# Kernel optimization log

Hardware: AMD Instinct MI355X
Metric: run time of the kernel (lower is better)

Reference implementation:

```python
import jax, jax.numpy as jnp
import numpy as np

NUM_UNITS = 64
NUM_NODES = 2048
COARSE_NODES = 256
INPUT_DIM = 1
BATCH = 64
AVG_DEGREE = 16


def _normalized_laplacian(adj):
    # A = A + I; L = D^-1/2 A^T D^-1/2 (matches scipy path in source)
    a = adj + np.eye(adj.shape[0], dtype=np.float64)
    d = a.sum(axis=1)
    d_inv_sqrt = np.power(d, -0.5)
    d_inv_sqrt[np.isinf(d_inv_sqrt)] = 0.0
    # (A @ D^-1/2).T @ D^-1/2 = A.T * d[:,None] * d[None,:]
    lap = a.T * d_inv_sqrt[:, None] * d_inv_sqrt[None, :]
    return lap.astype(np.float32)


def _random_adj(rng, n, deg):
    rows = np.repeat(np.arange(n), deg)
    cols = rng.integers(0, n, size=n * deg)
    a = np.zeros((n, n), dtype=np.float64)
    a[rows, cols] = 1.0
    a = np.maximum(a, a.T)  # symmetric
    np.fill_diagonal(a, 0.0)
    return a


def _xavier(key, shape):
    std = np.sqrt(2.0 / (shape[0] + shape[1]))
    return jax.random.normal(key, shape, dtype=jnp.float32) * std


def setup_inputs() -> dict:
    key = jax.random.key(0)
    ks = jax.random.split(key, 8)
    rng = np.random.default_rng(0)

    adj = jnp.asarray(_normalized_laplacian(_random_adj(rng, NUM_NODES, AVG_DEGREE)))
    adj1 = jnp.asarray(_normalized_laplacian(_random_adj(rng, COARSE_NODES, AVG_DEGREE)))
    # afc_mx in source is (num_nodes, coarse_nodes); afc = afc_mx.T, afct = afc_mx
    afc_mx = rng.random((NUM_NODES, COARSE_NODES)).astype(np.float32)
    afc = jnp.asarray(afc_mx.T)   # (C, N)
    afct = jnp.asarray(afc_mx)    # (N, C)

    in_size = INPUT_DIM + NUM_UNITS
    inputs = jax.random.normal(ks[0], (BATCH, NUM_NODES * INPUT_DIM), dtype=jnp.float32)
    state = jax.random.normal(ks[1], (BATCH, NUM_NODES * NUM_UNITS), dtype=jnp.float32)

    return {
        "inputs": inputs, "state": state,
        "adj": adj, "adj1": adj1, "afc": afc, "afct": afct,
        "w0": _xavier(ks[2], (in_size, 2 * NUM_UNITS)),
        "b0": jnp.zeros((2 * NUM_UNITS,), jnp.float32),
        "w1": _xavier(ks[3], (in_size, NUM_UNITS)),
        "b1": jnp.zeros((NUM_UNITS,), jnp.float32),
        "w01": _xavier(ks[4], (in_size, 2 * NUM_UNITS)),
        "b01": jnp.zeros((2 * NUM_UNITS,), jnp.float32),
        "w11": _xavier(ks[5], (in_size, NUM_UNITS)),
        "b11": jnp.zeros((NUM_UNITS,), jnp.float32),
    }


def _gc(inputs, state, adj, adj1, afc, afct, w, b, wf, bf):
    B = inputs.shape[0]
    N, C = adj.shape[0], adj1.shape[0]
    x = jnp.concatenate([inputs.reshape(B, N, -1), state.reshape(B, N, -1)], axis=2)
    F = x.shape[2]
    x0 = x.transpose(1, 2, 0).reshape(N, F * B)          # (N, F*B)
    x0fc = afc @ x0                                      # (C, F*B)
    x1 = adj @ x0                                        # graph conv, fine graph
    x1fc = adj1 @ x0fc                                   # graph conv, coarse graph
    x1 = x1 + jax.nn.sigmoid(afct @ x0fc)                # cross term fine<-coarse
    x1fc = x1fc + jax.nn.sigmoid(afc @ x1)               # cross term coarse<-fine
    out = x1.reshape(N, F, B).transpose(2, 0, 1).reshape(-1, F) @ w + b
    outfc = x1fc.reshape(C, F, B).transpose(2, 0, 1).reshape(-1, F) @ wf + bf
    return out.reshape(B, N, -1), outfc.reshape(B, C, -1)


def reference(inputs, state, adj, adj1, afc, afct, w0, b0, w1, b1, w01, b01, w11, b11):
    B = inputs.shape[0]
    N, U = NUM_NODES, NUM_UNITS
    x1, _x1fc = _gc(inputs, state, adj, adj1, afc, afct, w0, b0, w01, b01)
    value = jax.nn.sigmoid(x1)                           # (B, N, 2U)
    r, u = value[..., :U], value[..., U:]
    r = r.reshape(B, N * U)
    u = u.reshape(B, N * U)
    c0, _c1 = _gc(inputs, r * state, adj, adj1, afc, afct, w1, b1, w11, b11)
    c = jnp.tanh(c0).reshape(B, N * U)
    new_state = u * state + (1.0 - u) * c
    return new_state
```

## Files before the change

kernel.cpp:

```cpp
#include <hip/hip_runtime.h>
#include <hip/hip_bf16.h>
#include <math.h>

#define N_NODES 2048
#define C_NODES 256
#define BATCH   64
#define UNITS   64
#define JS      4096
#define NX      4160
#define JSX     4224
#define NU      131072
#define XSTR    4160
#define CAP     192

typedef short  s16x8 __attribute__((ext_vector_type(8)));
typedef float  f32x4 __attribute__((ext_vector_type(4)));

__device__ __forceinline__ float sigmoidf_(float x) { return 1.0f / (1.0f + __expf(-x)); }

__device__ __forceinline__ float bfs2f(short s) {
    union { float f; unsigned u; } w; w.u = ((unsigned)(unsigned short)s) << 16; return w.f;
}
__device__ __forceinline__ short f2bfs(float f) {
    __hip_bfloat16 h = __float2bfloat16(f);
    short s; __builtin_memcpy(&s, &h, 2); return s;
}

__device__ __forceinline__ void gload_lds16(const void* g, void* l) {
    __builtin_amdgcn_global_load_lds(
        (const __attribute__((address_space(1))) void*)g,
        (__attribute__((address_space(3))) void*)l, 16, 0, 0);
}

__global__ __launch_bounds__(256) void cvt_split(const float* __restrict__ s,
                                                 __hip_bfloat16* __restrict__ dh,
                                                 __hip_bfloat16* __restrict__ dl, int n)
{
    int stride = gridDim.x * 256;
    for (int i = blockIdx.x * 256 + threadIdx.x; i < n; i += stride) {
        float v = s[i];
        __hip_bfloat16 h = __float2bfloat16(v);
        dh[i] = h;
        dl[i] = __float2bfloat16(v - __bfloat162float(h));
    }
}

__global__ __launch_bounds__(256) void cvt_w(const float* __restrict__ w0,
                                             const float* __restrict__ w1,
                                             __hip_bfloat16* __restrict__ w0h, __hip_bfloat16* __restrict__ w0l,
                                             __hip_bfloat16* __restrict__ w1h, __hip_bfloat16* __restrict__ w1l)
{
    int stride = gridDim.x * 256;
    for (int e = blockIdx.x * 256 + threadIdx.x; e < 8192 + 4096; e += stride) {
        if (e < 8192) {
            int jj = e & 7, cell = e >> 3;
            int o = cell & 127, c = cell >> 7;
            float v = w0[(size_t)(1 + c * 8 + jj) * 128 + o];
            __hip_bfloat16 h = __float2bfloat16(v);
            w0h[e] = h; w0l[e] = __float2bfloat16(v - __bfloat162float(h));
        } else {
            int e2 = e - 8192;
            int jj = e2 & 7, cell = e2 >> 3;
            int o = cell & 63, c = cell >> 6;
            float v = w1[(size_t)(1 + c * 8 + jj) * 64 + o];
            __hip_bfloat16 h = __float2bfloat16(v);
            w1h[e2] = h; w1l[e2] = __float2bfloat16(v - __bfloat162float(h));
        }
    }
}

__global__ __launch_bounds__(256) void setup_ext(
    const float* __restrict__ inputs,
    __hip_bfloat16* __restrict__ xh, __hip_bfloat16* __restrict__ xl,
    __hip_bfloat16* __restrict__ fh, __hip_bfloat16* __restrict__ fl,
    __hip_bfloat16* __restrict__ X)
{
    int blk = blockIdx.x;
    if (blk < 64) {
        int b = blk;
        for (int n = threadIdx.x; n < N_NODES; n += 256) {
            float v = inputs[(size_t)b * N_NODES + n];
            __hip_bfloat16 h = __float2bfloat16(v);
            size_t o = (size_t)(JS + b) * N_NODES + n;
            xh[o] = h;
            xl[o] = __float2bfloat16(v - __bfloat162float(h));
            X[(size_t)n * XSTR + 4096 + b] = h;
        }
    } else {
        int r = NX + (blk - 64);
        __hip_bfloat16 z = __float2bfloat16(0.0f);
        for (int n = threadIdx.x; n < N_NODES; n += 256) {
            size_t o = (size_t)r * N_NODES + n;
            xh[o] = z; xl[o] = z;
        }
        for (int c = threadIdx.x; c < C_NODES; c += 256) {
            size_t o = (size_t)r * C_NODES + c;
            fh[o] = z; fl[o] = z;
        }
    }
}

__global__ __launch_bounds__(256) void build_csr(
    const float* __restrict__ adj,
    unsigned short* __restrict__ cols,
    float* __restrict__ vals,
    int* __restrict__ nnz)
{
    int row  = blockIdx.x * 4 + (threadIdx.x >> 6);
    int lane = threadIdx.x & 63;
    const float* a = adj + (size_t)row * N_NODES;
    int base = 0;
    for (int k0 = 0; k0 < N_NODES; k0 += 64) {
        float v = a[k0 + lane];
        unsigned long long m = __ballot(v != 0.0f);
        if (v != 0.0f) {
            int pos = base + __popcll(m & ((1ull << lane) - 1));
            if (pos < CAP) {
                cols[(size_t)row * CAP + pos] = (unsigned short)(k0 + lane);
                vals[(size_t)row * CAP + pos] = v;
            }
        }
        base += __popcll(m);
    }
    if (lane == 0) nnz[row] = base < CAP ? base : CAP;
}

__global__ __launch_bounds__(256) void build_x0sT(const float* __restrict__ st,
                                                  __hip_bfloat16* __restrict__ xh,
                                                  __hip_bfloat16* __restrict__ xl,
                                                  __hip_bfloat16* __restrict__ X)
{
    __shared__ float Ls[64 * 65];
    int n0 = blockIdx.x * 64;
    int b  = blockIdx.y;
    int t  = threadIdx.x;
    #pragma unroll
    for (int it = 0; it < 16; it++) {
        int idx = t + it * 256;
        int i = idx >> 6, u = idx & 63;
        float v = st[(size_t)b * NU + (size_t)(n0 + i) * 64 + u];
        Ls[i * 65 + u] = v;
        X[(size_t)(n0 + i) * XSTR + b * 64 + u] = __float2bfloat16(v);
    }
    __syncthreads();
    #pragma unroll
    for (int it = 0; it < 16; it++) {
        int idx = t + it * 256;
        int u = idx >> 6, i = idx & 63;
        float v = Ls[i * 65 + u];
        __hip_bfloat16 h = __float2bfloat16(v);
        size_t o = (size_t)(b * 64 + u) * N_NODES + n0 + i;
        xh[o] = h;
        xl[o] = __float2bfloat16(v - __bfloat162float(h));
    }
}

__global__ __launch_bounds__(256) void gemm1_split(
    const __hip_bfloat16* __restrict__ Ah, const __hip_bfloat16* __restrict__ Al,
    const __hip_bfloat16* __restrict__ Bh, const __hip_bfloat16* __restrict__ Bl,
    float* __restrict__ part)
{
    __shared__ __align__(16) __hip_bfloat16 AsH[4096];
    __shared__ __align__(16) __hip_bfloat16 AsL[4096];
    __shared__ __align__(16) __hip_bfloat16 BsH[4096];
    __shared__ __align__(16) __hip_bfloat16 BsL[4096];

    const int K = N_NODES;
    int tid  = threadIdx.x;
    int wave = tid >> 6, lane = tid & 63;
    int quad = lane >> 4, lr = lane & 15;
    int mBase = blockIdx.y * 64;
    int nBase = blockIdx.x * 64;
    int k0base = blockIdx.z * (K / 2);

    const __hip_bfloat16 *gAh[2], *gAl[2], *gBh[2], *gBl[2];
    __hip_bfloat16 *lAh[2], *lAl[2], *lBh[2], *lBl[2];
    #pragma unroll
    for (int ch = 0; ch < 2; ch++) {
        int cell = (wave * 2 + ch) * 64 + lane;
        int kb = cell >> 6, mm = cell & 63;
        size_t offA = (size_t)(mBase + mm) * K + k0base + kb * 8;
        size_t offB = (size_t)(nBase + mm) * K + k0base + kb * 8;
        gAh[ch] = Ah + offA; gAl[ch] = Al + offA;
        gBh[ch] = Bh + offB; gBl[ch] = Bl + offB;
        int lo = (wave * 2 + ch) * 512;
        lAh[ch] = AsH + lo; lAl[ch] = AsL + lo;
        lBh[ch] = BsH + lo; lBl[ch] = BsL + lo;
    }

    f32x4 acc[4];
    #pragma unroll
    for (int j = 0; j < 4; j++) { f32x4 z = {0.f,0.f,0.f,0.f}; acc[j] = z; }

    for (int k0 = 0; k0 < K / 2; k0 += 64) {
        #pragma unroll
        for (int ch = 0; ch < 2; ch++) {
            gload_lds16(gAh[ch] + k0, lAh[ch]);
            gload_lds16(gAl[ch] + k0, lAl[ch]);
            gload_lds16(gBh[ch] + k0, lBh[ch]);
            gload_lds16(gBl[ch] + k0, lBl[ch]);
        }
        __syncthreads();
        const s16x8* AhV = (const s16x8*)AsH;
        const s16x8* AlV = (const s16x8*)AsL;
        const s16x8* BhV = (const s16x8*)BsH;
        const s16x8* BlV = (const s16x8*)BsL;
        #pragma unroll
        for (int ks = 0; ks < 2; ks++) {
            int kb = ks * 4 + quad;
            s16x8 ah = AhV[kb * 64 + wave * 16 + lr];
            s16x8 al = AlV[kb * 64 + wave * 16 + lr];
            s16x8 bh[4], bl[4];
            #pragma unroll
            for (int j = 0; j < 4; j++) {
                bh[j] = BhV[kb * 64 + j * 16 + lr];
                bl[j] = BlV[kb * 64 + j * 16 + lr];
            }
            #pragma unroll
            for (int j = 0; j < 4; j++) {
                acc[j] = __builtin_amdgcn_mfma_f32_16x16x32_bf16(ah, bh[j], acc[j], 0, 0, 0);
                acc[j] = __builtin_amdgcn_mfma_f32_16x16x32_bf16(ah, bl[j], acc[j], 0, 0, 0);
                acc[j] = __builtin_amdgcn_mfma_f32_16x16x32_bf16(al, bh[j], acc[j], 0, 0, 0);
            }
        }
        __syncthreads();
    }

    float* dst = part + (size_t)blockIdx.z * NX * C_NODES;
    #pragma unroll
    for (int j = 0; j < 4; j++)
        #pragma unroll
        for (int r = 0; r < 4; r++) {
            int row = mBase + wave * 16 + quad * 4 + r;
            int col = nBase + j * 16 + lr;
            dst[(size_t)row * C_NODES + col] = acc[j][r];
        }
}

__global__ __launch_bounds__(256) void reduce_split(const float* __restrict__ part,
                                                    __hip_bfloat16* __restrict__ oh,
                                                    __hip_bfloat16* __restrict__ ol, int n)
{
    int stride = gridDim.x * 256;
    for (int i = blockIdx.x * 256 + threadIdx.x; i < n; i += stride) {
        float v = part[i] + part[(size_t)n + i];
        __hip_bfloat16 h = __float2bfloat16(v);
        oh[i] = h;
        ol[i] = __float2bfloat16(v - __bfloat162float(h));
    }
}

__global__ __launch_bounds__(256, 2) void gemm_coarse(
    const __hip_bfloat16* __restrict__ Ah, const __hip_bfloat16* __restrict__ Al,
    const __hip_bfloat16* __restrict__ Bh, const __hip_bfloat16* __restrict__ Bl,
    __hip_bfloat16* __restrict__ OutH, __hip_bfloat16* __restrict__ OutL)
{
    __shared__ __align__(16) __hip_bfloat16 S1[8192];
    __shared__ __align__(16) __hip_bfloat16 S2[8192];
    __shared__ __align__(16) __hip_bfloat16 S3[8192];
    __shared__ __align__(16) __hip_bfloat16 S4[8192];

    int tid  = threadIdx.x;
    int wave = tid >> 6, lane = tid & 63;
    int quad = lane >> 4, lr = lane & 15;
    int wr = wave >> 1, wc = wave & 1;
    int mBase = blockIdx.y * 128, nBase = blockIdx.x * 128;

    int cellkb[4], cellmm[4];
    #pragma unroll
    for (int ch = 0; ch < 4; ch++) {
        int cell = (wave * 4 + ch) * 64 + lane;
        cellkb[ch] = cell >> 7;
        cellmm[ch] = cell & 127;
    }

    f32x4 acc[4][4];
    #pragma unroll
    for (int i = 0; i < 4; i++)
        #pragma unroll
        for (int j = 0; j < 4; j++) { f32x4 z = {0.f,0.f,0.f,0.f}; acc[i][j] = z; }

    for (int k0 = 0; k0 < C_NODES; k0 += 64) {
        #pragma unroll
        for (int ch = 0; ch < 4; ch++) {
            size_t offA = (size_t)(mBase + cellmm[ch]) * C_NODES + k0 + cellkb[ch] * 8;
            size_t offB = (size_t)(nBase + cellmm[ch]) * C_NODES + k0 + cellkb[ch] * 8;
            int lo = (wave * 4 + ch) * 512;
            gload_lds16(Ah + offA, S1 + lo);
            gload_lds16(Al + offA, S2 + lo);
            gload_lds16(Bh + offB, S3 + lo);
            gload_lds16(Bl + offB, S4 + lo);
        }
        __syncthreads();
        const s16x8* AhV = (const s16x8*)S1;
        const s16x8* AlV = (const s16x8*)S2;
        const s16x8* BhV = (const s16x8*)S3;
        const s16x8* BlV = (const s16x8*)S4;
        #pragma unroll
        for (int ks = 0; ks < 2; ks++) {
            int kb = ks * 4 + quad;
            s16x8 ah[4], al[4], bh[4], bl[4];
            #pragma unroll
            for (int i = 0; i < 4; i++) {
                int idx = kb * 128 + wr * 64 + i * 16 + lr;
                ah[i] = AhV[idx]; al[i] = AlV[idx];
            }
            #pragma unroll
            for (int j = 0; j < 4; j++) {
                int idx = kb * 128 + wc * 64 + j * 16 + lr;
                bh[j] = BhV[idx]; bl[j] = BlV[idx];
            }
            #pragma unroll
            for (int i = 0; i < 4; i++)
                #pragma unroll
                for (int j = 0; j < 4; j++) {
                    acc[i][j] = __builtin_amdgcn_mfma_f32_16x16x32_bf16(ah[i], bh[j], acc[i][j], 0, 0, 0);
                    acc[i][j] = __builtin_amdgcn_mfma_f32_16x16x32_bf16(ah[i], bl[j], acc[i][j], 0, 0, 0);
                    acc[i][j] = __builtin_amdgcn_mfma_f32_16x16x32_bf16(al[i], bh[j], acc[i][j], 0, 0, 0);
                }
        }
        __syncthreads();
    }

    #pragma unroll
    for (int i = 0; i < 4; i++)
        #pragma unroll
        for (int j = 0; j < 4; j++)
            #pragma unroll
            for (int r = 0; r < 4; r++) {
                int row = mBase + wr * 64 + i * 16 + quad * 4 + r;
                int col = nBase + wc * 64 + j * 16 + lr;
                float v = sigmoidf_(acc[i][j][r]);
                size_t idx = (size_t)row * JSX + col;
                __hip_bfloat16 h = __float2bfloat16(v);
                OutH[idx] = h;
                OutL[idx] = __float2bfloat16(v - __bfloat162float(h));
            }
}

__global__ __launch_bounds__(256) void spmm_add(
    const __hip_bfloat16* __restrict__ X,
    const unsigned short* __restrict__ cols,
    const float* __restrict__ vals,
    const int* __restrict__ nnz,
    __hip_bfloat16* __restrict__ OutH,
    __hip_bfloat16* __restrict__ OutL)
{
    int wave = threadIdx.x >> 6, lane = threadIdx.x & 63;
    int n  = blockIdx.x * 4 + wave;
    int jt = blockIdx.y;
    int cnt = nnz[n];
    const unsigned short* cp = cols + (size_t)n * CAP;
    const float*          vp = vals + (size_t)n * CAP;
    const short* Xs = (const short*)X;

    if (jt < 8) {
        int j0 = jt * 512 + lane * 8;
        float acc[8];
        #pragma unroll
        for (int e = 0; e < 8; e++) acc[e] = 0.f;
        int i = 0;
        for (; i + 4 <= cnt; i += 4) {
            int   c0 = cp[i+0], c1 = cp[i+1], c2 = cp[i+2], c3 = cp[i+3];
            float a0 = vp[i+0], a1 = vp[i+1], a2 = vp[i+2], a3 = vp[i+3];
            s16x8 x0 = *(const s16x8*)(Xs + (size_t)c0 * XSTR + j0);
            s16x8 x1 = *(const s16x8*)(Xs + (size_t)c1 * XSTR + j0);
            s16x8 x2 = *(const s16x8*)(Xs + (size_t)c2 * XSTR + j0);
            s16x8 x3 = *(const s16x8*)(Xs + (size_t)c3 * XSTR + j0);
            #pragma unroll
            for (int e = 0; e < 8; e++)
                acc[e] += a0 * bfs2f(x0[e]) + a1 * bfs2f(x1[e])
                        + a2 * bfs2f(x2[e]) + a3 * bfs2f(x3[e]);
        }
        for (; i < cnt; i++) {
            int c = cp[i]; float a = vp[i];
            s16x8 xv = *(const s16x8*)(Xs + (size_t)c * XSTR + j0);
            #pragma unroll
            for (int e = 0; e < 8; e++) acc[e] += a * bfs2f(xv[e]);
        }
        size_t o = (size_t)n * JSX + jt * 512 + lane * 8;
        s16x8 h = *(const s16x8*)((const short*)OutH + o);
        s16x8 l = *(const s16x8*)((const short*)OutL + o);
        s16x8 nh, nl;
        #pragma unroll
        for (int e = 0; e < 8; e++) {
            float v = bfs2f(h[e]) + bfs2f(l[e]) + acc[e];
            short hh = f2bfs(v);
            nh[e] = hh;
            nl[e] = f2bfs(v - bfs2f(hh));
        }
        *(s16x8*)((short*)OutH + o) = nh;
        *(s16x8*)((short*)OutL + o) = nl;
    } else {
        float acc = 0.f;
        for (int i = 0; i < cnt; i++) {
            int c = cp[i]; float a = vp[i];
            acc += a * bfs2f(Xs[(size_t)c * XSTR + 4096 + lane]);
        }
        size_t o = (size_t)n * JSX + JS + lane;
        float v = bfs2f(((const short*)OutH)[o]) + bfs2f(((const short*)OutL)[o]) + acc;
        short hh = f2bfs(v);
        ((short*)OutH)[o] = hh;
        ((short*)OutL)[o] = f2bfs(v - bfs2f(hh));
    }
}

__global__ __launch_bounds__(256) void head1_mfma(
    const __hip_bfloat16* __restrict__ x1h, const __hip_bfloat16* __restrict__ x1l,
    const __hip_bfloat16* __restrict__ Wh, const __hip_bfloat16* __restrict__ Wl,
    const float* __restrict__ w0, const float* __restrict__ b0,
    const float* __restrict__ state,
    __hip_bfloat16* __restrict__ xh, __hip_bfloat16* __restrict__ xl,
    __hip_bfloat16* __restrict__ u_buf,
    __hip_bfloat16* __restrict__ Xout)
{
    __shared__ __align__(16) __hip_bfloat16 XsH[8192];
    __shared__ __align__(16) __hip_bfloat16 XsL[8192];
    __shared__ __align__(16) __hip_bfloat16 WhS[8192];
    __shared__ __align__(16) __hip_bfloat16 WlS[8192];
    __shared__ float xinS[128];

    int n0 = blockIdx.x * 128;
    int b  = blockIdx.y;
    int tid = threadIdx.x;
    int wave = tid >> 6, lane = tid & 63;
    int quad = lane >> 4, lr = lane & 15;
    int wr = wave >> 1, wc = wave & 1;

    #pragma unroll
    for (int ch = 0; ch < 4; ch++) {
        int idx = (wave * 4 + ch) * 64 + lane;
        int c = idx >> 7, n = idx & 127;
        size_t gx = (size_t)(n0 + n) * JSX + b * 64 + c * 8;
        gload_lds16(x1h + gx, XsH + (wave * 4 + ch) * 512);
        gload_lds16(x1l + gx, XsL + (wave * 4 + ch) * 512);
        gload_lds16(Wh + (size_t)idx * 8, WhS + (wave * 4 + ch) * 512);
        gload_lds16(Wl + (size_t)idx * 8, WlS + (wave * 4 + ch) * 512);
    }
    if (tid < 128) {
        size_t o = (size_t)(n0 + tid) * JSX + JS + b;
        xinS[tid] = __bfloat162float(x1h[o]) + __bfloat162float(x1l[o]);
    }
    __syncthreads();

    f32x4 acc[4][4];
    #pragma unroll
    for (int i = 0; i < 4; i++)
        #pragma unroll
        for (int j = 0; j < 4; j++) { f32x4 z = {0.f,0.f,0.f,0.f}; acc[i][j] = z; }

    const s16x8* XhV = (const s16x8*)XsH;
    const s16x8* XlV = (const s16x8*)XsL;
    const s16x8* WhV = (const s16x8*)WhS;
    const s16x8* WlV = (const s16x8*)WlS;
    #pragma unroll
    for (int ks = 0; ks < 2; ks++) {
        int kb = ks * 4 + quad;
        s16x8 ah[4], al[4], bh[4], bl[4];
        #pragma unroll
        for (int i = 0; i < 4; i++) {
            int idx = kb * 128 + wr * 64 + i * 16 + lr;
            ah[i] = XhV[idx]; al[i] = XlV[idx];
        }
        #pragma unroll
        for (int j = 0; j < 4; j++) {
            int idx = kb * 128 + wc * 64 + j * 16 + lr;
            bh[j] = WhV[idx]; bl[j] = WlV[idx];
        }
        #pragma unroll
        for (int i = 0; i < 4; i++)
            #pragma unroll
            for (int j = 0; j < 4; j++) {
                acc[i][j] = __builtin_amdgcn_mfma_f32_16x16x32_bf16(ah[i], bh[j], acc[i][j], 0, 0, 0);
                acc[i][j] = __builtin_amdgcn_mfma_f32_16x16x32_bf16(ah[i], bl[j], acc[i][j], 0, 0, 0);
                acc[i][j] = __builtin_amdgcn_mfma_f32_16x16x32_bf16(al[i], bh[j], acc[i][j], 0, 0, 0);
            }
    }
    __syncthreads();

    __hip_bfloat16* trH = XsH;
    __hip_bfloat16* trL = XsL;
    __hip_bfloat16* trX = WhS;

    #pragma unroll
    for (int i = 0; i < 4; i++)
        #pragma unroll
        for (int j = 0; j < 4; j++)
            #pragma unroll
            for (int r = 0; r < 4; r++) {
                int n_loc = wr * 64 + i * 16 + quad * 4 + r;
                int o = wc * 64 + j * 16 + lr;
                float g = acc[i][j][r] + w0[o] * xinS[n_loc] + b0[o];
                float sg = sigmoidf_(g);
                if (wc == 0) {
                    float sv = state[(size_t)b * NU + (size_t)(n0 + n_loc) * 64 + o];
                    float rs = sg * sv;
                    __hip_bfloat16 h = __float2bfloat16(rs);
                    trH[o * 128 + n_loc] = h;
                    trL[o * 128 + n_loc] = __float2bfloat16(rs - __bfloat162float(h));
                    trX[n_loc * 64 + o] = h;
                } else {
                    u_buf[(size_t)b * NU + (size_t)(n0 + n_loc) * 64 + (o - 64)] = __float2bfloat16(sg);
                }
            }
    __syncthreads();

    {
        int row = tid >> 2, seg = tid & 3;
        const uint4* sh = (const uint4*)(trH + row * 128 + seg * 32);
        const uint4* sl = (const uint4*)(trL + row * 128 + seg * 32);
        uint4* dh = (uint4*)(xh + (size_t)(b * 64 + row) * N_NODES + n0 + seg * 32);
        uint4* dl = (uint4*)(xl + (size_t)(b * 64 + row) * N_NODES + n0 + seg * 32);
        #pragma unroll
        for (int q = 0; q < 4; q++) { dh[q] = sh[q]; dl[q] = sl[q]; }
    }
    {
        int row2 = tid >> 1, half = tid & 1;
        const uint4* s = (const uint4*)(trX + row2 * 64 + half * 32);
        uint4* d = (uint4*)(Xout + (size_t)(n0 + row2) * XSTR + b * 64 + half * 32);
        #pragma unroll
        for (int q = 0; q < 4; q++) d[q] = s[q];
    }
}

__global__ __launch_bounds__(256) void head2_mfma(
    const __hip_bfloat16* __restrict__ x1h, const __hip_bfloat16* __restrict__ x1l,
    const __hip_bfloat16* __restrict__ Wh, const __hip_bfloat16* __restrict__ Wl,
    const float* __restrict__ w1, const float* __restrict__ b1,
    const float* __restrict__ state, const __hip_bfloat16* __restrict__ u_buf,
    float* __restrict__ out)
{
    __shared__ __align__(16) __hip_bfloat16 XsH[8192];
    __shared__ __align__(16) __hip_bfloat16 XsL[8192];
    __shared__ __align__(16) __hip_bfloat16 WhS[4096];
    __shared__ __align__(16) __hip_bfloat16 WlS[4096];
    __shared__ float xinS[128];

    int n0 = blockIdx.x * 128;
    int b  = blockIdx.y;
    int tid = threadIdx.x;
    int wave = tid >> 6, lane = tid & 63;
    int quad = lane >> 4, lr = lane & 15;

    #pragma unroll
    for (int ch = 0; ch < 4; ch++) {
        int idx = (wave * 4 + ch) * 64 + lane;
        int c = idx >> 7, n = idx & 127;
        size_t gx = (size_t)(n0 + n) * JSX + b * 64 + c * 8;
        gload_lds16(x1h + gx, XsH + (wave * 4 + ch) * 512);
        gload_lds16(x1l + gx, XsL + (wave * 4 + ch) * 512);
    }
    #pragma unroll
    for (int ch = 0; ch < 2; ch++) {
        int idx = (wave * 2 + ch) * 64 + lane;
        gload_lds16(Wh + (size_t)idx * 8, WhS + (wave * 2 + ch) * 512);
        gload_lds16(Wl + (size_t)idx * 8, WlS + (wave * 2 + ch) * 512);
    }
    if (tid < 128) {
        size_t o = (size_t)(n0 + tid) * JSX + JS + b;
        xinS[tid] = __bfloat162float(x1h[o]) + __bfloat162float(x1l[o]);
    }
    __syncthreads();

    f32x4 acc[2][4];
    #pragma unroll
    for (int i = 0; i < 2; i++)
        #pragma unroll
        for (int j = 0; j < 4; j++) { f32x4 z = {0.f,0.f,0.f,0.f}; acc[i][j] = z; }

    const s16x8* XhV = (const s16x8*)XsH;
    const s16x8* XlV = (const s16x8*)XsL;
    const s16x8* WhV = (const s16x8*)WhS;
    const s16x8* WlV = (const s16x8*)WlS;
    #pragma unroll
    for (int ks = 0; ks < 2; ks++) {
        int kb = ks * 4 + quad;
        s16x8 ah[2], al[2], bh[4], bl[4];
        #pragma unroll
        for (int i = 0; i < 2; i++) {
            int idx = kb * 128 + wave * 32 + i * 16 + lr;
            ah[i] = XhV[idx]; al[i] = XlV[idx];
        }
        #pragma unroll
        for (int j = 0; j < 4; j++) {
            int idx = kb * 64 + j * 16 + lr;
            bh[j] = WhV[idx]; bl[j] = WlV[idx];
        }
        #pragma unroll
        for (int i = 0; i < 2; i++)
            #pragma unroll
            for (int j = 0; j < 4; j++) {
                acc[i][j] = __builtin_amdgcn_mfma_f32_16x16x32_bf16(ah[i], bh[j], acc[i][j], 0, 0, 0);
                acc[i][j] = __builtin_amdgcn_mfma_f32_16x16x32_bf16(ah[i], bl[j], acc[i][j], 0, 0, 0);
                acc[i][j] = __builtin_amdgcn_mfma_f32_16x16x32_bf16(al[i], bh[j], acc[i][j], 0, 0, 0);
            }
    }

    #pragma unroll
    for (int i = 0; i < 2; i++)
        #pragma unroll
        for (int j = 0; j < 4; j++)
            #pragma unroll
            for (int r = 0; r < 4; r++) {
                int n_loc = wave * 32 + i * 16 + quad * 4 + r;
                int o = j * 16 + lr;
                float g = acc[i][j][r] + w1[o] * xinS[n_loc] + b1[o];
                float c = tanhf(g);
                size_t sidx = (size_t)b * NU + (size_t)(n0 + n_loc) * 64 + o;
                float ug = __bfloat162float(u_buf[sidx]);
                float sv = state[sidx];
                out[sidx] = ug * sv + (1.0f - ug) * c;
            }
}

extern "C" void kernel_launch(void* const* d_in, const int* in_sizes, int n_in,
                              void* d_out, int out_size, void* d_ws, size_t ws_size,
                              hipStream_t stream)
{
    const float* inputs = (const float*)d_in[0];
    const float* state  = (const float*)d_in[1];
    const float* adj    = (const float*)d_in[2];
    const float* afc    = (const float*)d_in[4];
    const float* afct   = (const float*)d_in[5];
    const float* w0     = (const float*)d_in[6];
    const float* b0     = (const float*)d_in[7];
    const float* w1     = (const float*)d_in[8];
    const float* b1     = (const float*)d_in[9];

    float* out = (float*)d_out;

    char* p = (char*)d_ws;
    __hip_bfloat16* afc_h    = (__hip_bfloat16*)p; p += (size_t)C_NODES * N_NODES * 2;
    __hip_bfloat16* afc_l    = (__hip_bfloat16*)p; p += (size_t)C_NODES * N_NODES * 2;
    __hip_bfloat16* afct_h   = (__hip_bfloat16*)p; p += (size_t)N_NODES * C_NODES * 2;
    __hip_bfloat16* afct_l   = (__hip_bfloat16*)p; p += (size_t)N_NODES * C_NODES * 2;
    __hip_bfloat16* w0T_h    = (__hip_bfloat16*)p; p += 8192 * 2;
    __hip_bfloat16* w0T_l    = (__hip_bfloat16*)p; p += 8192 * 2;
    __hip_bfloat16* w1T_h    = (__hip_bfloat16*)p; p += 4096 * 2;
    __hip_bfloat16* w1T_l    = (__hip_bfloat16*)p; p += 4096 * 2;
    __hip_bfloat16* x0sT_h   = (__hip_bfloat16*)p; p += (size_t)JSX * N_NODES * 2;
    __hip_bfloat16* x0sT_l   = (__hip_bfloat16*)p; p += (size_t)JSX * N_NODES * 2;
    __hip_bfloat16* x0fcT_h  = (__hip_bfloat16*)p; p += (size_t)JSX * C_NODES * 2;
    __hip_bfloat16* x0fcT_l  = (__hip_bfloat16*)p; p += (size_t)JSX * C_NODES * 2;
    __hip_bfloat16* x1s_h    = (__hip_bfloat16*)p; p += (size_t)N_NODES * JSX * 2;
    __hip_bfloat16* x1s_l    = (__hip_bfloat16*)p; p += (size_t)N_NODES * JSX * 2;
    __hip_bfloat16* u_buf    = (__hip_bfloat16*)p; p += (size_t)BATCH * NU * 2;
    float*          part     = (float*)p;          p += (size_t)2 * NX * C_NODES * 4;
    __hip_bfloat16* X        = (__hip_bfloat16*)p; p += (size_t)N_NODES * XSTR * 2;
    unsigned short* csr_cols = (unsigned short*)p; p += (size_t)N_NODES * CAP * 2;
    float*          csr_vals = (float*)p;          p += (size_t)N_NODES * CAP * 4;
    int*            csr_nnz  = (int*)p;            p += (size_t)N_NODES * 4;

    dim3 blk(256);

    cvt_split<<<256,  blk, 0, stream>>>(afc,  afc_h,  afc_l,  C_NODES * N_NODES);
    cvt_split<<<256,  blk, 0, stream>>>(afct, afct_h, afct_l, N_NODES * C_NODES);
    cvt_w    <<<32,   blk, 0, stream>>>(w0, w1, w0T_h, w0T_l, w1T_h, w1T_l);
    setup_ext<<<128,  blk, 0, stream>>>(inputs, x0sT_h, x0sT_l, x0fcT_h, x0fcT_l, X);
    build_csr<<<512,  blk, 0, stream>>>(adj, csr_cols, csr_vals, csr_nnz);

    build_x0sT<<<dim3(32, 64), blk, 0, stream>>>(state, x0sT_h, x0sT_l, X);
    gemm1_split<<<dim3(4, 65, 2), blk, 0, stream>>>(x0sT_h, x0sT_l, afc_h, afc_l, part);
    reduce_split<<<1024, blk, 0, stream>>>(part, x0fcT_h, x0fcT_l, NX * C_NODES);
    gemm_coarse<<<dim3(33, 16), blk, 0, stream>>>(afct_h, afct_l, x0fcT_h, x0fcT_l, x1s_h, x1s_l);
    spmm_add<<<dim3(512, 9), blk, 0, stream>>>(X, csr_cols, csr_vals, csr_nnz, x1s_h, x1s_l);
    head1_mfma<<<dim3(16, 64), blk, 0, stream>>>(x1s_h, x1s_l, w0T_h, w0T_l, w0, b0,
                                                 state, x0sT_h, x0sT_l, u_buf, X);

    gemm1_split<<<dim3(4, 65, 2), blk, 0, stream>>>(x0sT_h, x0sT_l, afc_h, afc_l, part);
    reduce_split<<<1024, blk, 0, stream>>>(part, x0fcT_h, x0fcT_l, NX * C_NODES);
    gemm_coarse<<<dim3(33, 16), blk, 0, stream>>>(afct_h, afct_l, x0fcT_h, x0fcT_l, x1s_h, x1s_l);
    spmm_add<<<dim3(512, 9), blk, 0, stream>>>(X, csr_cols, csr_vals, csr_nnz, x1s_h, x1s_l);
    head2_mfma<<<dim3(16, 64), blk, 0, stream>>>(x1s_h, x1s_l, w1T_h, w1T_l, w1, b1,
                                                 state, u_buf, out);
}
```

Measured before the change: 556.1 us.

## Store x1 in batch-major blocked layout and load MFMA operands directly from global

The intermediate x1 buffer is relaid out from node-major (N x JSX) to batch-blocked (66 x N x 64), so each head block reads a contiguous per-batch slab. The head kernels drop the LDS staging of X and weights and feed MFMA fragments with direct vector global loads. LDS use shrinks, which allows the launch bounds to request higher occupancy. The head1 transpose buffer gains an XOR swizzle to avoid bank conflicts, and Xout is written directly. The trade-off is that gemm_coarse and spmm_add now write with a more scattered stride, and weights are re-read from global or cache by every wave.

```diff
diff --git a/kernel.cpp b/kernel.cpp
--- a/kernel.cpp
+++ b/kernel.cpp
@@ -331,7 +331,7 @@
                 int row = mBase + wr * 64 + i * 16 + quad * 4 + r;
                 int col = nBase + wc * 64 + j * 16 + lr;
                 float v = sigmoidf_(acc[i][j][r]);
-                size_t idx = (size_t)row * JSX + col;
+                size_t idx = (size_t)(col >> 6) * NU + (size_t)row * 64 + (col & 63);
                 __hip_bfloat16 h = __float2bfloat16(v);
                 OutH[idx] = h;
                 OutL[idx] = __float2bfloat16(v - __bfloat162float(h));
@@ -378,7 +378,7 @@
             #pragma unroll
             for (int e = 0; e < 8; e++) acc[e] += a * bfs2f(xv[e]);
         }
-        size_t o = (size_t)n * JSX + jt * 512 + lane * 8;
+        size_t o = (size_t)(jt * 8 + (lane >> 3)) * NU + (size_t)n * 64 + (lane & 7) * 8;
         s16x8 h = *(const s16x8*)((const short*)OutH + o);
         s16x8 l = *(const s16x8*)((const short*)OutL + o);
         s16x8 nh, nl;
@@ -397,7 +397,7 @@
             int c = cp[i]; float a = vp[i];
             acc += a * bfs2f(Xs[(size_t)c * XSTR + 4096 + lane]);
         }
-        size_t o = (size_t)n * JSX + JS + lane;
+        size_t o = (size_t)64 * NU + (size_t)n * 64 + lane;
         float v = bfs2f(((const short*)OutH)[o]) + bfs2f(((const short*)OutL)[o]) + acc;
         short hh = f2bfs(v);
         ((short*)OutH)[o] = hh;
@@ -405,7 +405,7 @@
     }
 }
 
-__global__ __launch_bounds__(256) void head1_mfma(
+__global__ __launch_bounds__(256, 4) void head1_mfma(
     const __hip_bfloat16* __restrict__ x1h, const __hip_bfloat16* __restrict__ x1l,
     const __hip_bfloat16* __restrict__ Wh, const __hip_bfloat16* __restrict__ Wl,
     const float* __restrict__ w0, const float* __restrict__ b0,
@@ -414,10 +414,8 @@
     __hip_bfloat16* __restrict__ u_buf,
     __hip_bfloat16* __restrict__ Xout)
 {
-    __shared__ __align__(16) __hip_bfloat16 XsH[8192];
-    __shared__ __align__(16) __hip_bfloat16 XsL[8192];
-    __shared__ __align__(16) __hip_bfloat16 WhS[8192];
-    __shared__ __align__(16) __hip_bfloat16 WlS[8192];
+    __shared__ __align__(16) short trH[8192];
+    __shared__ __align__(16) short trL[8192];
     __shared__ float xinS[128];
 
     int n0 = blockIdx.x * 128;
@@ -427,60 +425,45 @@
     int quad = lane >> 4, lr = lane & 15;
     int wr = wave >> 1, wc = wave & 1;
 
-    #pragma unroll
-    for (int ch = 0; ch < 4; ch++) {
-        int idx = (wave * 4 + ch) * 64 + lane;
-        int c = idx >> 7, n = idx & 127;
-        size_t gx = (size_t)(n0 + n) * JSX + b * 64 + c * 8;
-        gload_lds16(x1h + gx, XsH + (wave * 4 + ch) * 512);
-        gload_lds16(x1l + gx, XsL + (wave * 4 + ch) * 512);
-        gload_lds16(Wh + (size_t)idx * 8, WhS + (wave * 4 + ch) * 512);
-        gload_lds16(Wl + (size_t)idx * 8, WlS + (wave * 4 + ch) * 512);
-    }
     if (tid < 128) {
-        size_t o = (size_t)(n0 + tid) * JSX + JS + b;
+        size_t o = (size_t)64 * NU + (size_t)(n0 + tid) * 64 + b;
         xinS[tid] = __bfloat162float(x1h[o]) + __bfloat162float(x1l[o]);
     }
+
+    f32x4 acc[4][4];
+    #pragma unroll
+    for (int i = 0; i < 4; i++)
+        #pragma unroll
+        for (int j = 0; j < 4; j++) { f32x4 z = {0.f,0.f,0.f,0.f}; acc[i][j] = z; }
+
+    const short* Xh = (const short*)x1h + (size_t)b * NU;
+    const short* Xl = (const short*)x1l + (size_t)b * NU;
+    const short* Wh_ = (const short*)Wh;
+    const short* Wl_ = (const short*)Wl;
+
+    #pragma unroll
+    for (int ks = 0; ks < 2; ks++) {
+        s16x8 ah[4], al[4];
+        #pragma unroll
+        for (int i = 0; i < 4; i++) {
+            size_t off = (size_t)(n0 + wr * 64 + i * 16 + lr) * 64 + ks * 32 + quad * 8;
+            ah[i] = *(const s16x8*)(Xh + off);
+            al[i] = *(const s16x8*)(Xl + off);
+        }
+        #pragma unroll
+        for (int j = 0; j < 4; j++) {
+            size_t wo = ((size_t)(ks * 4 + quad) * 128 + wc * 64 + j * 16 + lr) * 8;
+            s16x8 bh = *(const s16x8*)(Wh_ + wo);
+            s16x8 bl = *(const s16x8*)(Wl_ + wo);
+            #pragma unroll
+            for (int i = 0; i < 4; i++) {
+                acc[i][j] = __builtin_amdgcn_mfma_f32_16x16x32_bf16(ah[i], bh, acc[i][j], 0, 0, 0);
+                acc[i][j] = __builtin_amdgcn_mfma_f32_16x16x32_bf16(ah[i], bl, acc[i][j], 0, 0, 0);
+                acc[i][j] = __builtin_amdgcn_mfma_f32_16x16x32_bf16(al[i], bh, acc[i][j], 0, 0, 0);
+            }
+        }
+    }
     __syncthreads();
-
-    f32x4 acc[4][4];
-    #pragma unroll
-    for (int i = 0; i < 4; i++)
-        #pragma unroll
-        for (int j = 0; j < 4; j++) { f32x4 z = {0.f,0.f,0.f,0.f}; acc[i][j] = z; }
-
-    const s16x8* XhV = (const s16x8*)XsH;
-    const s16x8* XlV = (const s16x8*)XsL;
-    const s16x8* WhV = (const s16x8*)WhS;
-    const s16x8* WlV = (const s16x8*)WlS;
-    #pragma unroll
-    for (int ks = 0; ks < 2; ks++) {
-        int kb = ks * 4 + quad;
-        s16x8 ah[4], al[4], bh[4], bl[4];
-        #pragma unroll
-        for (int i = 0; i < 4; i++) {
-            int idx = kb * 128 + wr * 64 + i * 16 + lr;
-            ah[i] = XhV[idx]; al[i] = XlV[idx];
-        }
-        #pragma unroll
-        for (int j = 0; j < 4; j++) {
-            int idx = kb * 128 + wc * 64 + j * 16 + lr;
-            bh[j] = WhV[idx]; bl[j] = WlV[idx];
-        }
-        #pragma unroll
-        for (int i = 0; i < 4; i++)
-            #pragma unroll
-            for (int j = 0; j < 4; j++) {
-                acc[i][j] = __builtin_amdgcn_mfma_f32_16x16x32_bf16(ah[i], bh[j], acc[i][j], 0, 0, 0);
-                acc[i][j] = __builtin_amdgcn_mfma_f32_16x16x32_bf16(ah[i], bl[j], acc[i][j], 0, 0, 0);
-                acc[i][j] = __builtin_amdgcn_mfma_f32_16x16x32_bf16(al[i], bh[j], acc[i][j], 0, 0, 0);
-            }
-    }
-    __syncthreads();
-
-    __hip_bfloat16* trH = XsH;
-    __hip_bfloat16* trL = XsL;
-    __hip_bfloat16* trX = WhS;
 
     #pragma unroll
     for (int i = 0; i < 4; i++)
@@ -495,10 +478,11 @@
                 if (wc == 0) {
                     float sv = state[(size_t)b * NU + (size_t)(n0 + n_loc) * 64 + o];
                     float rs = sg * sv;
-                    __hip_bfloat16 h = __float2bfloat16(rs);
-                    trH[o * 128 + n_loc] = h;
-                    trL[o * 128 + n_loc] = __float2bfloat16(rs - __bfloat162float(h));
-                    trX[n_loc * 64 + o] = h;
+                    short h = f2bfs(rs);
+                    int sw = n_loc ^ ((o & 15) << 3);
+                    trH[o * 128 + sw] = h;
+                    trL[o * 128 + sw] = f2bfs(rs - bfs2f(h));
+                    ((short*)Xout)[(size_t)(n0 + n_loc) * XSTR + b * 64 + o] = h;
                 } else {
                     u_buf[(size_t)b * NU + (size_t)(n0 + n_loc) * 64 + (o - 64)] = __float2bfloat16(sg);
                 }
@@ -507,33 +491,25 @@
 
     {
         int row = tid >> 2, seg = tid & 3;
-        const uint4* sh = (const uint4*)(trH + row * 128 + seg * 32);
-        const uint4* sl = (const uint4*)(trL + row * 128 + seg * 32);
-        uint4* dh = (uint4*)(xh + (size_t)(b * 64 + row) * N_NODES + n0 + seg * 32);
-        uint4* dl = (uint4*)(xl + (size_t)(b * 64 + row) * N_NODES + n0 + seg * 32);
-        #pragma unroll
-        for (int q = 0; q < 4; q++) { dh[q] = sh[q]; dl[q] = sl[q]; }
-    }
-    {
-        int row2 = tid >> 1, half = tid & 1;
-        const uint4* s = (const uint4*)(trX + row2 * 64 + half * 32);
-        uint4* d = (uint4*)(Xout + (size_t)(n0 + row2) * XSTR + b * 64 + half * 32);
-        #pragma unroll
-        for (int q = 0; q < 4; q++) d[q] = s[q];
-    }
-}
-
-__global__ __launch_bounds__(256) void head2_mfma(
+        int xorv = (row & 15) << 3;
+        short* dh = (short*)xh + (size_t)(b * 64 + row) * N_NODES + n0 + seg * 32;
+        short* dl = (short*)xl + (size_t)(b * 64 + row) * N_NODES + n0 + seg * 32;
+        #pragma unroll
+        for (int q = 0; q < 4; q++) {
+            int src = row * 128 + ((seg * 32 + q * 8) ^ xorv);
+            *(uint4*)(dh + q * 8) = *(const uint4*)(trH + src);
+            *(uint4*)(dl + q * 8) = *(const uint4*)(trL + src);
+        }
+    }
+}
+
+__global__ __launch_bounds__(256, 4) void head2_mfma(
     const __hip_bfloat16* __restrict__ x1h, const __hip_bfloat16* __restrict__ x1l,
     const __hip_bfloat16* __restrict__ Wh, const __hip_bfloat16* __restrict__ Wl,
     const float* __restrict__ w1, const float* __restrict__ b1,
     const float* __restrict__ state, const __hip_bfloat16* __restrict__ u_buf,
     float* __restrict__ out)
 {
-    __shared__ __align__(16) __hip_bfloat16 XsH[8192];
-    __shared__ __align__(16) __hip_bfloat16 XsL[8192];
-    __shared__ __align__(16) __hip_bfloat16 WhS[4096];
-    __shared__ __align__(16) __hip_bfloat16 WlS[4096];
     __shared__ float xinS[128];
 
     int n0 = blockIdx.x * 128;
@@ -542,59 +518,45 @@
     int wave = tid >> 6, lane = tid & 63;
     int quad = lane >> 4, lr = lane & 15;
 
-    #pragma unroll
-    for (int ch = 0; ch < 4; ch++) {
-        int idx = (wave * 4 + ch) * 64 + lane;
-        int c = idx >> 7, n = idx & 127;
-        size_t gx = (size_t)(n0 + n) * JSX + b * 64 + c * 8;
-        gload_lds16(x1h + gx, XsH + (wave * 4 + ch) * 512);
-        gload_lds16(x1l + gx, XsL + (wave * 4 + ch) * 512);
-    }
-    #pragma unroll
-    for (int ch = 0; ch < 2; ch++) {
-        int idx = (wave * 2 + ch) * 64 + lane;
-        gload_lds16(Wh + (size_t)idx * 8, WhS + (wave * 2 + ch) * 512);
-        gload_lds16(Wl + (size_t)idx * 8, WlS + (wave * 2 + ch) * 512);
-    }
     if (tid < 128) {
-        size_t o = (size_t)(n0 + tid) * JSX + JS + b;
+        size_t o = (size_t)64 * NU + (size_t)(n0 + tid) * 64 + b;
         xinS[tid] = __bfloat162float(x1h[o]) + __bfloat162float(x1l[o]);
     }
+
+    f32x4 acc[2][4];
+    #pragma unroll
+    for (int i = 0; i < 2; i++)
+        #pragma unroll
+        for (int j = 0; j < 4; j++) { f32x4 z = {0.f,0.f,0.f,0.f}; acc[i][j] = z; }
+
+    const short* Xh = (const short*)x1h + (size_t)b * NU;
+    const short* Xl = (const short*)x1l + (size_t)b * NU;
+    const short* Wh_ = (const short*)Wh;
+    const short* Wl_ = (const short*)Wl;
+
+    #pragma unroll
+    for (int ks = 0; ks < 2; ks++) {
+        s16x8 ah[2], al[2];
+        #pragma unroll
+        for (int i = 0; i < 2; i++) {
+            size_t off = (size_t)(n0 + wave * 32 + i * 16 + lr) * 64 + ks * 32 + quad * 8;
+            ah[i] = *(const s16x8*)(Xh + off);
+            al[i] = *(const s16x8*)(Xl + off);
+        }
+        #pragma unroll
+        for (int j = 0; j < 4; j++) {
+            size_t wo = ((size_t)(ks * 4 + quad) * 64 + j * 16 + lr) * 8;
+            s16x8 bh = *(const s16x8*)(Wh_ + wo);
+            s16x8 bl = *(const s16x8*)(Wl_ + wo);
+            #pragma unroll
+            for (int i = 0; i < 2; i++) {
+                acc[i][j] = __builtin_amdgcn_mfma_f32_16x16x32_bf16(ah[i], bh, acc[i][j], 0, 0, 0);
+                acc[i][j] = __builtin_amdgcn_mfma_f32_16x16x32_bf16(ah[i], bl, acc[i][j], 0, 0, 0);
+                acc[i][j] = __builtin_amdgcn_mfma_f32_16x16x32_bf16(al[i], bh, acc[i][j], 0, 0, 0);
+            }
+        }
+    }
     __syncthreads();
-
-    f32x4 acc[2][4];
-    #pragma unroll
-    for (int i = 0; i < 2; i++)
-        #pragma unroll
-        for (int j = 0; j < 4; j++) { f32x4 z = {0.f,0.f,0.f,0.f}; acc[i][j] = z; }
-
-    const s16x8* XhV = (const s16x8*)XsH;
-    const s16x8* XlV = (const s16x8*)XsL;
-    const s16x8* WhV = (const s16x8*)WhS;
-    const s16x8* WlV = (const s16x8*)WlS;
-    #pragma unroll
-    for (int ks = 0; ks < 2; ks++) {
-        int kb = ks * 4 + quad;
-        s16x8 ah[2], al[2], bh[4], bl[4];
-        #pragma unroll
-        for (int i = 0; i < 2; i++) {
-            int idx = kb * 128 + wave * 32 + i * 16 + lr;
-            ah[i] = XhV[idx]; al[i] = XlV[idx];
-        }
-        #pragma unroll
-        for (int j = 0; j < 4; j++) {
-            int idx = kb * 64 + j * 16 + lr;
-            bh[j] = WhV[idx]; bl[j] = WlV[idx];
-        }
-        #pragma unroll
-        for (int i = 0; i < 2; i++)
-            #pragma unroll
-            for (int j = 0; j < 4; j++) {
-                acc[i][j] = __builtin_amdgcn_mfma_f32_16x16x32_bf16(ah[i], bh[j], acc[i][j], 0, 0, 0);
-                acc[i][j] = __builtin_amdgcn_mfma_f32_16x16x32_bf16(ah[i], bl[j], acc[i][j], 0, 0, 0);
-                acc[i][j] = __builtin_amdgcn_mfma_f32_16x16x32_bf16(al[i], bh[j], acc[i][j], 0, 0, 0);
-            }
-    }
 
     #pragma unroll
     for (int i = 0; i < 2; i++)
@@ -642,8 +604,8 @@
     __hip_bfloat16* x0sT_l   = (__hip_bfloat16*)p; p += (size_t)JSX * N_NODES * 2;
     __hip_bfloat16* x0fcT_h  = (__hip_bfloat16*)p; p += (size_t)JSX * C_NODES * 2;
     __hip_bfloat16* x0fcT_l  = (__hip_bfloat16*)p; p += (size_t)JSX * C_NODES * 2;
-    __hip_bfloat16* x1s_h    = (__hip_bfloat16*)p; p += (size_t)N_NODES * JSX * 2;
-    __hip_bfloat16* x1s_l    = (__hip_bfloat16*)p; p += (size_t)N_NODES * JSX * 2;
+    __hip_bfloat16* x1B_h    = (__hip_bfloat16*)p; p += (size_t)66 * NU * 2;
+    __hip_bfloat16* x1B_l    = (__hip_bfloat16*)p; p += (size_t)66 * NU * 2;
     __hip_bfloat16* u_buf    = (__hip_bfloat16*)p; p += (size_t)BATCH * NU * 2;
     float*          part     = (float*)p;          p += (size_t)2 * NX * C_NODES * 4;
     __hip_bfloat16* X        = (__hip_bfloat16*)p; p += (size_t)N_NODES * XSTR * 2;
@@ -662,15 +624,15 @@
     build_x0sT<<<dim3(32, 64), blk, 0, stream>>>(state, x0sT_h, x0sT_l, X);
     gemm1_split<<<dim3(4, 65, 2), blk, 0, stream>>>(x0sT_h, x0sT_l, afc_h, afc_l, part);
     reduce_split<<<1024, blk, 0, stream>>>(part, x0fcT_h, x0fcT_l, NX * C_NODES);
-    gemm_coarse<<<dim3(33, 16), blk, 0, stream>>>(afct_h, afct_l, x0fcT_h, x0fcT_l, x1s_h, x1s_l);
-    spmm_add<<<dim3(512, 9), blk, 0, stream>>>(X, csr_cols, csr_vals, csr_nnz, x1s_h, x1s_l);
-    head1_mfma<<<dim3(16, 64), blk, 0, stream>>>(x1s_h, x1s_l, w0T_h, w0T_l, w0, b0,
+    gemm_coarse<<<dim3(33, 16), blk, 0, stream>>>(afct_h, afct_l, x0fcT_h, x0fcT_l, x1B_h, x1B_l);
+    spmm_add<<<dim3(512, 9), blk, 0, stream>>>(X, csr_cols, csr_vals, csr_nnz, x1B_h, x1B_l);
+    head1_mfma<<<dim3(16, 64), blk, 0, stream>>>(x1B_h, x1B_l, w0T_h, w0T_l, w0, b0,
                                                  state, x0sT_h, x0sT_l, u_buf, X);
 
     gemm1_split<<<dim3(4, 65, 2), blk, 0, stream>>>(x0sT_h, x0sT_l, afc_h, afc_l, part);
     reduce_split<<<1024, blk, 0, stream>>>(part, x0fcT_h, x0fcT_l, NX * C_NODES);
-    gemm_coarse<<<dim3(33, 16), blk, 0, stream>>>(afct_h, afct_l, x0fcT_h, x0fcT_l, x1s_h, x1s_l);
-    spmm_add<<<dim3(512, 9), blk, 0, stream>>>(X, csr_cols, csr_vals, csr_nnz, x1s_h, x1s_l);
-    head2_mfma<<<dim3(16, 64), blk, 0, stream>>>(x1s_h, x1s_l, w1T_h, w1T_l, w1, b1,
+    gemm_coarse<<<dim3(33, 16), blk, 0, stream>>>(afct_h, afct_l, x0fcT_h, x0fcT_l, x1B_h, x1B_l);
+    spmm_add<<<dim3(512, 9), blk, 0, stream>>>(X, csr_cols, csr_vals, csr_nnz, x1B_h, x1B_l);
+    head2_mfma<<<dim3(16, 64), blk, 0, stream>>>(x1B_h, x1B_l, w1T_h, w1T_l, w1, b1,
                                                  state, u_buf, out);
 }
```

Result: faster. 529.9 us (-4.7%).
